# Kernel tuning notes

Hardware: AMD Instinct MI355X
Metric: run time of the kernel (lower is better)

Reference implementation:

```python
import jax, jax.numpy as jnp
import numpy as np

D = 256       # in_channels == hd_channels
H = 8         # heads
HC = D // H   # head dim = 32
NV = 30000    # variables
NC = 60000    # clauses
E = 120000    # edges per polarity


def setup_inputs() -> dict:
    key = jax.random.key(0)
    ks = jax.random.split(key, 16)
    std = 0.02
    v = jax.random.normal(ks[0], (NV, D), jnp.float32)
    c = jax.random.normal(ks[1], (NC, D), jnp.float32)
    # adj row0 indexes clauses (c), row1 indexes variables (v)
    adj_pos = jnp.stack([jax.random.randint(ks[2], (E,), 0, NC),
                         jax.random.randint(ks[3], (E,), 0, NV)]).astype(jnp.int32)
    adj_neg = jnp.stack([jax.random.randint(ks[4], (E,), 0, NC),
                         jax.random.randint(ks[5], (E,), 0, NV)]).astype(jnp.int32)
    # shared projections (ModuleList([lin]*2) shares one module)
    Wq = jax.random.normal(ks[6], (D, D), jnp.float32) * std
    bq = jnp.zeros((D,), jnp.float32)
    Wkv = jax.random.normal(ks[7], (D, 2 * D), jnp.float32) * std
    bkv = jnp.zeros((2 * D,), jnp.float32)
    ffn_v_w1 = jax.random.normal(ks[8], (D, D), jnp.float32) * std
    ffn_v_b1 = jnp.zeros((D,), jnp.float32)
    ffn_v_w2 = jax.random.normal(ks[9], (D, D), jnp.float32) * std
    ffn_v_b2 = jnp.zeros((D,), jnp.float32)
    ffn_c_w1 = jax.random.normal(ks[10], (D, D), jnp.float32) * std
    ffn_c_b1 = jnp.zeros((D,), jnp.float32)
    ffn_c_w2 = jax.random.normal(ks[11], (D, D), jnp.float32) * std
    ffn_c_b2 = jnp.zeros((D,), jnp.float32)
    ones = jnp.ones((D,), jnp.float32)
    zeros = jnp.zeros((D,), jnp.float32)
    return dict(v=v, c=c, adj_pos=adj_pos, adj_neg=adj_neg,
                Wq=Wq, bq=bq, Wkv=Wkv, bkv=bkv,
                ffn_v_w1=ffn_v_w1, ffn_v_b1=ffn_v_b1, ffn_v_w2=ffn_v_w2, ffn_v_b2=ffn_v_b2,
                ffn_c_w1=ffn_c_w1, ffn_c_b1=ffn_c_b1, ffn_c_w2=ffn_c_w2, ffn_c_b2=ffn_c_b2,
                ln_att_v_g=ones, ln_att_v_b=zeros, ln_ffn_v_g=ones, ln_ffn_v_b=zeros,
                ln_att_c_g=ones, ln_att_c_b=zeros, ln_ffn_c_g=ones, ln_ffn_c_b=zeros)


def _split(x):
    return x.reshape(x.shape[0], H, HC)


def _ln(x, g, b, eps=1e-5):
    m = jnp.mean(x, axis=-1, keepdims=True)
    va = jnp.mean(jnp.square(x - m), axis=-1, keepdims=True)
    return (x - m) * jax.lax.rsqrt(va + eps) * g + b


def _seg_softmax(x, seg, n):
    m = jax.ops.segment_max(x, seg, num_segments=n)      # (n, H)
    e = jnp.exp(x - m[seg])
    s = jax.ops.segment_sum(e, seg, num_segments=n)
    return e / s[seg]


def _sparse_attn(q, k, val, e_q, e_k, n_q):
    # q: (Lq,H,HC); k,val: (Lk,H,HC); per-edge dot -> segment softmax -> scatter aggregate
    qk = jnp.einsum('ehc,ehc->eh', q[e_q], k[e_k]) * (1.0 / np.sqrt(HC))
    alpha = _seg_softmax(qk, e_q, n_q)                   # (E,H)
    return jax.ops.segment_sum(alpha[:, :, None] * val[e_k], e_q, num_segments=n_q)


def _cross(x, y, adj, Wq, bq, Wkv, bkv):
    # adj[0] indexes y, adj[1] indexes x
    ey, ex = adj[0], adj[1]
    qx = _split(x @ Wq + bq)
    ky, vy = jnp.split(y @ Wkv + bkv, 2, axis=-1)
    w = _sparse_attn(qx, _split(ky), _split(vy), ex, ey, x.shape[0])   # x queries, transposed edges
    qy = _split(y @ Wq + bq)
    kx, vx = jnp.split(x @ Wkv + bkv, 2, axis=-1)
    u = _sparse_attn(qy, _split(kx), _split(vx), ey, ex, y.shape[0])   # y queries
    return w.reshape(x.shape[0], D), u.reshape(y.shape[0], D)


def _ffn(x, w1, b1, w2, b2):
    return jax.nn.gelu(x @ w1 + b1, approximate=False) @ w2 + b2


def reference(v, c, adj_pos, adj_neg, Wq, bq, Wkv, bkv,
              ffn_v_w1, ffn_v_b1, ffn_v_w2, ffn_v_b2,
              ffn_c_w1, ffn_c_b1, ffn_c_w2, ffn_c_b2,
              ln_att_v_g, ln_att_v_b, ln_ffn_v_g, ln_ffn_v_b,
              ln_att_c_g, ln_att_c_b, ln_ffn_c_g, ln_ffn_c_b):
    wp, up = _cross(v, c, adj_pos, Wq, bq, Wkv, bkv)
    wn, un = _cross(v, c, adj_neg, Wq, bq, Wkv, bkv)
    v1 = _ln(v + (wp + wn), ln_att_v_g, ln_att_v_b)
    c1 = _ln(c + (up + un), ln_att_c_g, ln_att_c_b)
    v2 = _ln(v1 + _ffn(v1, ffn_v_w1, ffn_v_b1, ffn_v_w2, ffn_v_b2), ln_ffn_v_g, ln_ffn_v_b)
    c2 = _ln(c1 + _ffn(c1, ffn_c_w1, ffn_c_b1, ffn_c_w2, ffn_c_b2), ln_ffn_c_g, ln_ffn_c_b)
    return (v2, c2)
```

## Files before the change

### kernel.cpp

```cpp
#include <hip/hip_runtime.h>
#include <math.h>

#define DD 256
#define NH 8

typedef __attribute__((ext_vector_type(8))) short short8;
typedef __attribute__((ext_vector_type(4))) float floatx4;

__device__ __forceinline__ float b2f(unsigned short u) {
    return __uint_as_float(((unsigned)u) << 16);
}
__device__ __forceinline__ unsigned short f2b(float f) {
    unsigned u = __float_as_uint(f);
    return (unsigned short)((u + 0x7fffu + ((u >> 16) & 1u)) >> 16);
}

__device__ __forceinline__ void gload_lds16(const void* g, void* l) {
    __builtin_amdgcn_global_load_lds(
        (const __attribute__((address_space(1))) void*)g,
        (__attribute__((address_space(3))) void*)l, 16, 0, 0);
}

__global__ void detect_dtype(const unsigned* __restrict__ ones_words, int* __restrict__ flag) {
    flag[0] = (ones_words[0] == 0x3F800000u) ? 0 : 1;
}

__device__ __forceinline__ void load8(const void* base, size_t off, int f32, unsigned short* dst) {
    if (f32) {
        const float4* p = (const float4*)((const float*)base + off);
        float4 x = p[0], y = p[1];
        dst[0] = f2b(x.x); dst[1] = f2b(x.y); dst[2] = f2b(x.z); dst[3] = f2b(x.w);
        dst[4] = f2b(y.x); dst[5] = f2b(y.y); dst[6] = f2b(y.z); dst[7] = f2b(y.w);
    } else {
        *(uint4*)dst = *(const uint4*)((const unsigned short*)base + off);
    }
}

__global__ void wt_build(const void* __restrict__ Wq, const void* __restrict__ Wkv,
                         const void* __restrict__ f1v, const void* __restrict__ f1c,
                         const void* __restrict__ f2v, const void* __restrict__ f2c,
                         short* __restrict__ wt, const int* __restrict__ flagp)
{
    const int extf = (*flagp == 0);
    const void* src; int N; size_t dst0;
    switch (blockIdx.z) {
        case 0:  src = Wq;  N = 256; dst0 = 0;          break;
        case 1:  src = Wkv; N = 512; dst0 = 256 * 256;  break;
        case 2:  src = f1v; N = 256; dst0 = 768 * 256;  break;
        case 3:  src = f1c; N = 256; dst0 = 1024 * 256; break;
        case 4:  src = f2v; N = 256; dst0 = 1280 * 256; break;
        default: src = f2c; N = 256; dst0 = 1536 * 256; break;
    }
    int n0 = blockIdx.x * 32, k0 = blockIdx.y * 32;
    if (n0 >= N) return;
    __shared__ short tile[32][33];
    int tx = threadIdx.x & 31, ty = threadIdx.x >> 5;
    #pragma unroll
    for (int i = 0; i < 32; i += 8) {
        int k = k0 + ty + i, n = n0 + tx;
        float val = extf ? ((const float*)src)[(size_t)k * N + n]
                         : b2f(((const unsigned short*)src)[(size_t)k * N + n]);
        tile[ty + i][tx] = (short)f2b(val);
    }
    __syncthreads();
    #pragma unroll
    for (int i = 0; i < 32; i += 8)
        wt[dst0 + (size_t)(n0 + ty + i) * 256 + k0 + tx] = tile[tx][ty + i];
}


__device__ __forceinline__ void stage_b256(const short* wtp, int nbase, int ksub,
                                           char* dstbuf, int wave, int lane)
{
    const char* wb = (const char*)wtp;
    int b = lane & 7;
    #pragma unroll
    for (int i = 0; i < 4; ++i) {
        int r = i * 64 + wave * 8 + (lane >> 3);
        size_t src = (size_t)(nbase + r) * 512 + (size_t)ksub * 128
                   + (size_t)((b * 16) ^ ((r & 7) << 4));
        gload_lds16(wb + src, dstbuf + i * 8192 + wave * 1024);
    }
}

__launch_bounds__(512, 2)
__global__ void proj_gemm5(const void* __restrict__ va, const void* __restrict__ ca,
                           int NVr, int NCr, int bv,
                           const short* __restrict__ wt,
                           const void* __restrict__ bq, const void* __restrict__ bkv,
                           unsigned short* __restrict__ qbuf, unsigned short* __restrict__ kvbuf,
                           const int* __restrict__ flagp)
{
    __shared__ __align__(16) short As[128][264];
    __shared__ __align__(16) char Bs[2][256 * 128];
    const int extf = (*flagp == 0);
    const int t = threadIdx.x;
    const int wave = t >> 6, lane = t & 63;
    const int wm = wave >> 2, wn = wave & 3;
    const int fr = lane & 15, fq = lane >> 4;
    const int bx = blockIdx.x;
    int grow0, nrows, abase_row; const void* asrc;
    if (bx < bv) { grow0 = bx * 128; asrc = va; abase_row = grow0; nrows = NVr - grow0; }
    else { int mc0 = (bx - bv) * 128; grow0 = NVr + mc0; asrc = ca; abase_row = mc0; nrows = NCr - mc0; }
    if (nrows > 128) nrows = 128;

    stage_b256(wt, 0, 0, Bs[0], wave, lane);
    {
        int rbase = t >> 3, cslot = t & 7;
        #pragma unroll
        for (int ii = 0; ii < 8; ++ii) {
            int row = rbase + (ii >> 2) * 64;
            int col = (cslot + (ii & 3) * 8) * 8;
            __align__(16) unsigned short a8[8] = {0, 0, 0, 0, 0, 0, 0, 0};
            if (row < nrows) load8(asrc, (size_t)(abase_row + row) * DD + col, extf, a8);
            *(uint4*)(&As[row][col]) = *(const uint4*)a8;
        }
    }
    __syncthreads();

    int cur = 0;
    for (int c = 0; c < 3; ++c) {
        floatx4 acc[4][4] = {};
        #pragma unroll
        for (int s = 0; s < 4; ++s) {
            int tt = c * 4 + s;
            if (tt + 1 < 12)
                stage_b256(wt, ((tt + 1) >> 2) * 256, (tt + 1) & 3, Bs[cur ^ 1], wave, lane);
            const char* bcur = Bs[cur];
            #pragma unroll
            for (int k32 = 0; k32 < 2; ++k32) {
                short8 afv[4], bfv[4];
                #pragma unroll
                for (int m = 0; m < 4; ++m)
                    afv[m] = *(const short8*)(&As[wm * 64 + m * 16 + fr][s * 64 + k32 * 32 + fq * 8]);
                #pragma unroll
                for (int j = 0; j < 4; ++j) {
                    int rn = wn * 64 + j * 16 + fr;
                    int kb = (k32 * 64 + fq * 16) ^ ((rn & 7) << 4);
                    bfv[j] = *(const short8*)(bcur + rn * 128 + kb);
                }
                #pragma unroll
                for (int m = 0; m < 4; ++m)
                    #pragma unroll
                    for (int j = 0; j < 4; ++j)
                        acc[m][j] = __builtin_amdgcn_mfma_f32_16x16x32_bf16(afv[m], bfv[j], acc[m][j], 0, 0, 0);
            }
            __syncthreads();
            cur ^= 1;
        }
        unsigned short* outp; int ldo, colb; const void* bias;
        if (c == 0) { outp = qbuf;  ldo = 256; colb = 0;             bias = bq;  }
        else        { outp = kvbuf; ldo = 512; colb = (c - 1) * 256; bias = bkv; }
        #pragma unroll
        for (int j = 0; j < 4; ++j) {
            int col = colb + wn * 64 + j * 16 + fr;
            float bvv = extf ? ((const float*)bias)[col] : b2f(((const unsigned short*)bias)[col]);
            #pragma unroll
            for (int m = 0; m < 4; ++m) {
                #pragma unroll
                for (int r = 0; r < 4; ++r) {
                    int rr = wm * 64 + m * 16 + fq * 4 + r;
                    if (rr < nrows)
                        outp[(size_t)(grow0 + rr) * ldo + col] = f2b(acc[m][j][r] + bvv);
                }
            }
        }
    }
}

template<int EPI>
__launch_bounds__(512, 2)
__global__ void ffn_gemm5(const unsigned short* __restrict__ A,
                          int NVr, int NCr, int bv,
                          const short* __restrict__ wtV, const short* __restrict__ wtC,
                          const void* __restrict__ biasV, const void* __restrict__ biasC,
                          void* __restrict__ outp, const int* __restrict__ flagp)
{
    __shared__ __align__(16) short As[128][264];
    __shared__ __align__(16) char Bs[2][256 * 128];
    const int extf = (*flagp == 0);
    const int t = threadIdx.x;
    const int wave = t >> 6, lane = t & 63;
    const int wm = wave >> 2, wn = wave & 3;
    const int fr = lane & 15, fq = lane >> 4;
    const int bx = blockIdx.x;
    int grow0, nrows; const short* wtp; const void* bias;
    if (bx < bv) { grow0 = bx * 128; nrows = NVr - grow0; wtp = wtV; bias = biasV; }
    else { grow0 = NVr + (bx - bv) * 128; nrows = NVr + NCr - grow0; wtp = wtC; bias = biasC; }
    if (nrows > 128) nrows = 128;

    stage_b256(wtp, 0, 0, Bs[0], wave, lane);
    {
        int rbase = t >> 3, cslot = t & 7;
        #pragma unroll
        for (int ii = 0; ii < 8; ++ii) {
            int row = rbase + (ii >> 2) * 64;
            int col = (cslot + (ii & 3) * 8) * 8;
            uint4 a8 = make_uint4(0u, 0u, 0u, 0u);
            if (row < nrows) a8 = *(const uint4*)(A + (size_t)(grow0 + row) * DD + col);
            *(uint4*)(&As[row][col]) = a8;
        }
    }
    __syncthreads();

    int cur = 0;
    floatx4 acc[4][4] = {};
    #pragma unroll
    for (int s = 0; s < 4; ++s) {
        if (s + 1 < 4)
            stage_b256(wtp, 0, s + 1, Bs[cur ^ 1], wave, lane);
        const char* bcur = Bs[cur];
        #pragma unroll
        for (int k32 = 0; k32 < 2; ++k32) {
            short8 afv[4], bfv[4];
            #pragma unroll
            for (int m = 0; m < 4; ++m)
                afv[m] = *(const short8*)(&As[wm * 64 + m * 16 + fr][s * 64 + k32 * 32 + fq * 8]);
            #pragma unroll
            for (int j = 0; j < 4; ++j) {
                int rn = wn * 64 + j * 16 + fr;
                int kb = (k32 * 64 + fq * 16) ^ ((rn & 7) << 4);
                bfv[j] = *(const short8*)(bcur + rn * 128 + kb);
            }
            #pragma unroll
            for (int m = 0; m < 4; ++m)
                #pragma unroll
                for (int j = 0; j < 4; ++j)
                    acc[m][j] = __builtin_amdgcn_mfma_f32_16x16x32_bf16(afv[m], bfv[j], acc[m][j], 0, 0, 0);
        }
        __syncthreads();
        cur ^= 1;
    }
    #pragma unroll
    for (int j = 0; j < 4; ++j) {
        int col = wn * 64 + j * 16 + fr;
        float bvv = extf ? ((const float*)bias)[col] : b2f(((const unsigned short*)bias)[col]);
        #pragma unroll
        for (int m = 0; m < 4; ++m) {
            #pragma unroll
            for (int r = 0; r < 4; ++r) {
                int rr = wm * 64 + m * 16 + fq * 4 + r;
                if (rr < nrows) {
                    float x = acc[m][j][r] + bvv;
                    if (EPI == 1) {
                        x = 0.5f * x * (1.0f + erff(x * 0.70710678118654752f));
                        ((unsigned short*)outp)[(size_t)(grow0 + rr) * DD + col] = f2b(x);
                    } else {
                        ((float*)outp)[(size_t)(grow0 + rr) * DD + col] = x;
                    }
                }
            }
        }
    }
}

__global__ void csr_count(const int* __restrict__ ap, const int* __restrict__ an,
                          int E, int NV, int NT, int* __restrict__ counts) {
    int e = blockIdx.x * 256 + threadIdx.x;
    if (e >= E) return;
    atomicAdd(&counts[ap[E + e]], 1);
    atomicAdd(&counts[NV + ap[e]], 1);
    atomicAdd(&counts[NT + an[E + e]], 1);
    atomicAdd(&counts[NT + NV + an[e]], 1);
}

__global__ void scan_block(const int* __restrict__ counts, int* __restrict__ offs,
                           int* __restrict__ bsum, int n) {
    __shared__ int sm[256];
    int i = blockIdx.x * 256 + threadIdx.x;
    int x = (i < n) ? counts[i] : 0;
    sm[threadIdx.x] = x;
    __syncthreads();
    #pragma unroll
    for (int d = 1; d < 256; d <<= 1) {
        int t = (threadIdx.x >= d) ? sm[threadIdx.x - d] : 0;
        __syncthreads();
        sm[threadIdx.x] += t;
        __syncthreads();
    }
    if (i < n) offs[i] = sm[threadIdx.x] - x;
    if (threadIdx.x == 255) bsum[blockIdx.x] = sm[255];
}

__global__ void scan_bsum(int* __restrict__ bsum, int nb) {
    __shared__ int sm[256];
    __shared__ int carry;
    if (threadIdx.x == 0) carry = 0;
    __syncthreads();
    for (int base = 0; base < nb; base += 256) {
        int i = base + threadIdx.x;
        int x = (i < nb) ? bsum[i] : 0;
        sm[threadIdx.x] = x;
        __syncthreads();
        #pragma unroll
        for (int d = 1; d < 256; d <<= 1) {
            int t = (threadIdx.x >= d) ? sm[threadIdx.x - d] : 0;
            __syncthreads();
            sm[threadIdx.x] += t;
            __syncthreads();
        }
        int excl = sm[threadIdx.x] - x + carry;
        if (i < nb) bsum[i] = excl;
        __syncthreads();
        if (threadIdx.x == 0) carry += sm[255];
        __syncthreads();
    }
}

__global__ void scan_add(int* __restrict__ offs, const int* __restrict__ bsum, int n) {
    int i = blockIdx.x * 256 + threadIdx.x;
    if (i < n) offs[i] += bsum[blockIdx.x];
}

__global__ void csr_fill(const int* __restrict__ ap, const int* __restrict__ an,
                         int E, int NV, int NT, int* __restrict__ offs, int* __restrict__ eids) {
    int e = blockIdx.x * 256 + threadIdx.x;
    if (e >= E) return;
    int p;
    p = atomicAdd(&offs[ap[E + e]], 1);            eids[p] = e * 2;
    p = atomicAdd(&offs[NV + ap[e]], 1);           eids[p] = e * 2 + 1;
    p = atomicAdd(&offs[NT + an[E + e]], 1);       eids[p] = e * 2;
    p = atomicAdd(&offs[NT + NV + an[e]], 1);      eids[p] = e * 2 + 1;
}

__launch_bounds__(256)
__global__ void edge_logits(const int* __restrict__ adj, int E, int NV,
                            const unsigned short* __restrict__ qbuf,
                            const unsigned short* __restrict__ kvbuf,
                            float* __restrict__ qk)
{
    int t = blockIdx.x * 256 + threadIdx.x;
    if (t >= E * 16) return;
    int e = t >> 4, rem = t & 15;
    int dir = rem >> 3, h = rem & 7;
    int ce = adj[e], xe = adj[E + e];
    int qrow = dir ? (NV + ce) : xe;
    int krow = dir ? xe : (NV + ce);
    const unsigned short* qp = qbuf + (size_t)qrow * DD + h * 32;
    const unsigned short* kp = kvbuf + (size_t)krow * 512 + h * 32;
    float s = 0.f;
    #pragma unroll
    for (int i = 0; i < 4; ++i) {
        uint4 qv = ((const uint4*)qp)[i];
        uint4 kv = ((const uint4*)kp)[i];
        const unsigned short* qa = (const unsigned short*)&qv;
        const unsigned short* ka = (const unsigned short*)&kv;
        #pragma unroll
        for (int j = 0; j < 8; ++j) s += b2f(qa[j]) * b2f(ka[j]);
    }
    qk[t] = s * 0.17677669529663689f;
}

__launch_bounds__(256)
__global__ void seg_attn(const int* __restrict__ offs_end, const int* __restrict__ counts,
                         const int* __restrict__ eids, const int* __restrict__ adj,
                         int E, int NV, const float* __restrict__ qk,
                         const unsigned short* __restrict__ kvbuf,
                         float* __restrict__ osum, int NT, int acc_mode)
{
    int seg = blockIdx.x * 4 + (threadIdx.x >> 6);
    if (seg >= NT) return;
    int lane = threadIdx.x & 63;
    int deg = counts[seg];
    float4* op = (float4*)(osum + (size_t)seg * DD) + lane;
    if (deg == 0) {
        if (!acc_mode) *op = make_float4(0.f, 0.f, 0.f, 0.f);
        return;
    }
    int beg = offs_end[seg] - deg;
    int slot = lane >> 3, h = lane & 7;
    float m = -1e30f;
    for (int j = slot; j < deg; j += 8)
        m = fmaxf(m, qk[(size_t)eids[beg + j] * 8 + h]);
    m = fmaxf(m, __shfl_xor(m, 8));
    m = fmaxf(m, __shfl_xor(m, 16));
    m = fmaxf(m, __shfl_xor(m, 32));
    float s = 0.f;
    for (int j = slot; j < deg; j += 8)
        s += __expf(qk[(size_t)eids[beg + j] * 8 + h] - m);
    s += __shfl_xor(s, 8);
    s += __shfl_xor(s, 16);
    s += __shfl_xor(s, 32);
    int h3 = lane >> 3;
    float m3 = __shfl(m, h3);
    float rs3 = 1.f / __shfl(s, h3);
    float a0 = 0.f, a1 = 0.f, a2 = 0.f, a3 = 0.f;
    for (int j = 0; j < deg; ++j) {
        int eid = eids[beg + j];
        int e = eid >> 1, dir = eid & 1;
        int krow = dir ? adj[E + e] : (NV + adj[e]);
        float alpha = __expf(qk[(size_t)eid * 8 + h3] - m3) * rs3;
        ushort4 vv = *(const ushort4*)(kvbuf + (size_t)krow * 512 + DD + lane * 4);
        a0 += alpha * b2f(vv.x);
        a1 += alpha * b2f(vv.y);
        a2 += alpha * b2f(vv.z);
        a3 += alpha * b2f(vv.w);
    }
    float4 o;
    if (acc_mode) {
        float4 old = *op;
        o.x = old.x + a0; o.y = old.y + a1; o.z = old.z + a2; o.w = old.w + a3;
    } else {
        o.x = a0; o.y = a1; o.z = a2; o.w = a3;
    }
    *op = o;
}

template<int BASE_EXT, int OUT_EXT>
__launch_bounds__(256)
__global__ void ln_res(const void* __restrict__ baseA, const void* __restrict__ baseB,
                       const float* __restrict__ add,
                       const void* __restrict__ gA, const void* __restrict__ bA,
                       const void* __restrict__ gB, const void* __restrict__ bB,
                       void* __restrict__ out, int NA, int Ntot, const int* __restrict__ flagp)
{
    int row = blockIdx.x * 4 + (threadIdx.x >> 6);
    if (row >= Ntot) return;
    int lane = threadIdx.x & 63;
    const int extf = (*flagp == 0);
    const void *base, *g, *b;
    size_t roff;
    if (row < NA) { base = baseA; g = gA; b = bA; roff = (size_t)row * DD; }
    else          { base = baseB; g = gB; b = bB; roff = (size_t)(row - NA) * DD; }
    float4 a = ((const float4*)(add + (size_t)row * DD))[lane];
    float y0, y1, y2, y3;
    if (BASE_EXT && extf) {
        float4 t = ((const float4*)((const float*)base + roff))[lane];
        y0 = t.x; y1 = t.y; y2 = t.z; y3 = t.w;
    } else {
        ushort4 t = ((const ushort4*)((const unsigned short*)base + roff))[lane];
        y0 = b2f(t.x); y1 = b2f(t.y); y2 = b2f(t.z); y3 = b2f(t.w);
    }
    y0 += a.x; y1 += a.y; y2 += a.z; y3 += a.w;
    float s = y0 + y1 + y2 + y3;
    #pragma unroll
    for (int off = 32; off; off >>= 1) s += __shfl_xor(s, off);
    float mean = s * (1.0f / DD);
    float d0 = y0 - mean, d1 = y1 - mean, d2 = y2 - mean, d3 = y3 - mean;
    float v = d0 * d0 + d1 * d1 + d2 * d2 + d3 * d3;
    #pragma unroll
    for (int off = 32; off; off >>= 1) v += __shfl_xor(v, off);
    float rstd = rsqrtf(v * (1.0f / DD) + 1e-5f);
    float g0, g1, g2, g3, t0, t1, t2, t3;
    if (extf) {
        float4 gg = ((const float4*)g)[lane]; float4 bt = ((const float4*)b)[lane];
        g0 = gg.x; g1 = gg.y; g2 = gg.z; g3 = gg.w;
        t0 = bt.x; t1 = bt.y; t2 = bt.z; t3 = bt.w;
    } else {
        ushort4 gg = ((const ushort4*)g)[lane]; ushort4 bt = ((const ushort4*)b)[lane];
        g0 = b2f(gg.x); g1 = b2f(gg.y); g2 = b2f(gg.z); g3 = b2f(gg.w);
        t0 = b2f(bt.x); t1 = b2f(bt.y); t2 = b2f(bt.z); t3 = b2f(bt.w);
    }
    float o0 = d0 * rstd * g0 + t0, o1 = d1 * rstd * g1 + t1;
    float o2 = d2 * rstd * g2 + t2, o3 = d3 * rstd * g3 + t3;
    if (OUT_EXT && extf) {
        float4 o; o.x = o0; o.y = o1; o.z = o2; o.w = o3;
        ((float4*)((float*)out + (size_t)row * DD))[lane] = o;
    } else {
        ushort4 o;
        o.x = f2b(o0); o.y = f2b(o1); o.z = f2b(o2); o.w = f2b(o3);
        ((ushort4*)((unsigned short*)out + (size_t)row * DD))[lane] = o;
    }
}

extern "C" void kernel_launch(void* const* d_in, const int* in_sizes, int n_in,
                              void* d_out, int out_size, void* d_ws, size_t ws_size,
                              hipStream_t stream)
{
    const void* v   = d_in[0];
    const void* c   = d_in[1];
    const int* adj_pos = (const int*)d_in[2];
    const int* adj_neg = (const int*)d_in[3];
    const void* Wq  = d_in[4];
    const void* bq  = d_in[5];
    const void* Wkv = d_in[6];
    const void* bkv = d_in[7];
    const void* fvw1 = d_in[8];
    const void* fvb1 = d_in[9];
    const void* fvw2 = d_in[10];
    const void* fvb2 = d_in[11];
    const void* fcw1 = d_in[12];
    const void* fcb1 = d_in[13];
    const void* fcw2 = d_in[14];
    const void* fcb2 = d_in[15];
    const void* lavg = d_in[16];
    const void* lavb = d_in[17];
    const void* lfvg = d_in[18];
    const void* lfvb = d_in[19];
    const void* lacg = d_in[20];
    const void* lacb = d_in[21];
    const void* lfcg = d_in[22];
    const void* lfcb = d_in[23];

    const int NV = in_sizes[0] / DD;
    const int NC = in_sizes[1] / DD;
    const int NT = NV + NC;
    const int E  = in_sizes[2] / 2;

    char* w = (char*)d_ws;
    int* flagp = (int*)w;
    size_t off = 256;
    float* osum = (float*)(w + off);
    off += (size_t)NT * DD * 4;
    unsigned short* qbuf = (unsigned short*)(w + off);
    off += (size_t)NT * DD * 2;
    unsigned short* kvbuf = (unsigned short*)(w + off);
    off += (size_t)NT * DD * 4;
    float* qkbuf = (float*)(w + off);
    off += (size_t)E * 16 * 4;
    int* counts = (int*)(w + off);
    off += (size_t)2 * NT * 4;
    int* offs = (int*)(w + off);
    off += (size_t)2 * NT * 4;
    int* eids = (int*)(w + off);
    off += (size_t)4 * E * 4;
    int* bsum = (int*)(w + off);
    off += 4096;
    short* wt = (short*)(w + off);

    dim3 blk(256), blk512(512);
    const int bv = (NV + 127) / 128, bc = (NC + 127) / 128;
    const int nbE = (E + 255) / 256;
    const int n2 = 2 * NT, nb2 = (n2 + 255) / 256;

    detect_dtype<<<dim3(1), dim3(1), 0, stream>>>((const unsigned*)lavg, flagp);
    wt_build<<<dim3(16, 8, 6), blk, 0, stream>>>(Wq, Wkv, fvw1, fcw1, fvw2, fcw2, wt, flagp);

    proj_gemm5<<<dim3(bv + bc), blk512, 0, stream>>>(v, c, NV, NC, bv, wt, bq, bkv,
                                                     qbuf, kvbuf, flagp);

    hipMemsetAsync(counts, 0, (size_t)n2 * 4, stream);
    csr_count<<<dim3(nbE), blk, 0, stream>>>(adj_pos, adj_neg, E, NV, NT, counts);
    scan_block<<<dim3(nb2), blk, 0, stream>>>(counts, offs, bsum, n2);
    scan_bsum<<<dim3(1), blk, 0, stream>>>(bsum, nb2);
    scan_add<<<dim3(nb2), blk, 0, stream>>>(offs, bsum, n2);
    csr_fill<<<dim3(nbE), blk, 0, stream>>>(adj_pos, adj_neg, E, NV, NT, offs, eids);

    for (int p = 0; p < 2; ++p) {
        const int* adj = p ? adj_neg : adj_pos;
        edge_logits<<<dim3((E * 16 + 255) / 256), blk, 0, stream>>>(adj, E, NV, qbuf, kvbuf, qkbuf);
        seg_attn<<<dim3((NT + 3) / 4), blk, 0, stream>>>(offs + (size_t)p * NT, counts + (size_t)p * NT,
                                                         eids, adj, E, NV, qkbuf, kvbuf, osum, NT, p);
    }

    unsigned short* x1 = qbuf;
    ln_res<1, 0><<<dim3((NT + 3) / 4), blk, 0, stream>>>(v, c, osum, lavg, lavb, lacg, lacb,
                                                         x1, NV, NT, flagp);

    unsigned short* hbuf = kvbuf;
    ffn_gemm5<1><<<dim3(bv + bc), blk512, 0, stream>>>(x1, NV, NC, bv,
                                                       wt + (size_t)768 * 256, wt + (size_t)1024 * 256,
                                                       fvb1, fcb1, hbuf, flagp);
    ffn_gemm5<2><<<dim3(bv + bc), blk512, 0, stream>>>(hbuf, NV, NC, bv,
                                                       wt + (size_t)1280 * 256, wt + (size_t)1536 * 256,
                                                       fvb2, fcb2, osum, flagp);

    ln_res<0, 1><<<dim3((NT + 3) / 4), blk, 0, stream>>>(x1, x1 + (size_t)NV * DD, osum,
                                                         lfvg, lfvb, lfcg, lfcb,
                                                         d_out, NV, NT, flagp);
}
```

Measured before the change: 754.1 us.

## Shrink GEMM tiles to 64 rows with 4 waves and single-buffered XOR-swizzled LDS

The projection and FFN GEMMs now use 64-row tiles with 256 threads instead of 128-row tiles with 512 threads. Each wave covers all 64 rows against its own 64-column slice. The B buffer drops double buffering: the next slice is staged only after a barrier. The A tile gets an XOR swizzle instead of padding, and the MFMA operand order is swapped so each lane holds 4 consecutive columns, allowing vectorized bias loads and packed 8/16-byte stores. The aim is more blocks for occupancy and tail balance and cheaper epilogue stores, at the cost of losing the load/compute overlap from double buffering and staging the weights twice as often per row.

```diff
diff --git a/kernel.cpp b/kernel.cpp
--- a/kernel.cpp
+++ b/kernel.cpp
@@ -69,99 +69,108 @@
 }
 
 
-__device__ __forceinline__ void stage_b256(const short* wtp, int nbase, int ksub,
-                                           char* dstbuf, int wave, int lane)
+__device__ __forceinline__ void stage_b256w4(const short* wtp, int nbase, int ksub,
+                                             char* dstbuf, int wave, int lane)
 {
     const char* wb = (const char*)wtp;
     int b = lane & 7;
     #pragma unroll
-    for (int i = 0; i < 4; ++i) {
-        int r = i * 64 + wave * 8 + (lane >> 3);
+    for (int i = 0; i < 8; ++i) {
+        int r = i * 32 + wave * 8 + (lane >> 3);
         size_t src = (size_t)(nbase + r) * 512 + (size_t)ksub * 128
                    + (size_t)((b * 16) ^ ((r & 7) << 4));
-        gload_lds16(wb + src, dstbuf + i * 8192 + wave * 1024);
-    }
-}
-
-__launch_bounds__(512, 2)
-__global__ void proj_gemm5(const void* __restrict__ va, const void* __restrict__ ca,
+        gload_lds16(wb + src, dstbuf + i * 4096 + wave * 1024);
+    }
+}
+
+__launch_bounds__(256, 2)
+__global__ void proj_gemm7(const void* __restrict__ va, const void* __restrict__ ca,
                            int NVr, int NCr, int bv,
                            const short* __restrict__ wt,
                            const void* __restrict__ bq, const void* __restrict__ bkv,
                            unsigned short* __restrict__ qbuf, unsigned short* __restrict__ kvbuf,
                            const int* __restrict__ flagp)
 {
-    __shared__ __align__(16) short As[128][264];
-    __shared__ __align__(16) char Bs[2][256 * 128];
+    __shared__ __align__(16) char As[64 * 512];
+    __shared__ __align__(16) char Bs[256 * 128];
     const int extf = (*flagp == 0);
     const int t = threadIdx.x;
     const int wave = t >> 6, lane = t & 63;
-    const int wm = wave >> 2, wn = wave & 3;
     const int fr = lane & 15, fq = lane >> 4;
     const int bx = blockIdx.x;
     int grow0, nrows, abase_row; const void* asrc;
-    if (bx < bv) { grow0 = bx * 128; asrc = va; abase_row = grow0; nrows = NVr - grow0; }
-    else { int mc0 = (bx - bv) * 128; grow0 = NVr + mc0; asrc = ca; abase_row = mc0; nrows = NCr - mc0; }
-    if (nrows > 128) nrows = 128;
-
-    stage_b256(wt, 0, 0, Bs[0], wave, lane);
+    if (bx < bv) { grow0 = bx * 64; asrc = va; abase_row = grow0; nrows = NVr - grow0; }
+    else { int mc0 = (bx - bv) * 64; grow0 = NVr + mc0; asrc = ca; abase_row = mc0; nrows = NCr - mc0; }
+    if (nrows > 64) nrows = 64;
+
+    stage_b256w4(wt, 0, 0, Bs, wave, lane);
     {
-        int rbase = t >> 3, cslot = t & 7;
+        int row = t >> 2, cslot = t & 3;
         #pragma unroll
         for (int ii = 0; ii < 8; ++ii) {
-            int row = rbase + (ii >> 2) * 64;
-            int col = (cslot + (ii & 3) * 8) * 8;
+            int colb = cslot * 16 + ii * 64;
+            int swz = colb ^ ((row & 7) << 4);
             __align__(16) unsigned short a8[8] = {0, 0, 0, 0, 0, 0, 0, 0};
-            if (row < nrows) load8(asrc, (size_t)(abase_row + row) * DD + col, extf, a8);
-            *(uint4*)(&As[row][col]) = *(const uint4*)a8;
-        }
-    }
-    __syncthreads();
-
-    int cur = 0;
+            if (row < nrows) load8(asrc, (size_t)(abase_row + row) * DD + colb / 2, extf, a8);
+            *(uint4*)(As + row * 512 + swz) = *(const uint4*)a8;
+        }
+    }
+
+    int tt = 0;
     for (int c = 0; c < 3; ++c) {
         floatx4 acc[4][4] = {};
         #pragma unroll
-        for (int s = 0; s < 4; ++s) {
-            int tt = c * 4 + s;
-            if (tt + 1 < 12)
-                stage_b256(wt, ((tt + 1) >> 2) * 256, (tt + 1) & 3, Bs[cur ^ 1], wave, lane);
-            const char* bcur = Bs[cur];
+        for (int s = 0; s < 4; ++s, ++tt) {
+            __syncthreads();
             #pragma unroll
             for (int k32 = 0; k32 < 2; ++k32) {
                 short8 afv[4], bfv[4];
                 #pragma unroll
-                for (int m = 0; m < 4; ++m)
-                    afv[m] = *(const short8*)(&As[wm * 64 + m * 16 + fr][s * 64 + k32 * 32 + fq * 8]);
+                for (int m = 0; m < 4; ++m) {
+                    int row = m * 16 + fr;
+                    int byt = (s * 128 + k32 * 64 + fq * 16) ^ ((row & 7) << 4);
+                    afv[m] = *(const short8*)(As + row * 512 + byt);
+                }
                 #pragma unroll
                 for (int j = 0; j < 4; ++j) {
-                    int rn = wn * 64 + j * 16 + fr;
+                    int rn = wave * 64 + j * 16 + fr;
                     int kb = (k32 * 64 + fq * 16) ^ ((rn & 7) << 4);
-                    bfv[j] = *(const short8*)(bcur + rn * 128 + kb);
+                    bfv[j] = *(const short8*)(Bs + rn * 128 + kb);
                 }
                 #pragma unroll
                 for (int m = 0; m < 4; ++m)
                     #pragma unroll
                     for (int j = 0; j < 4; ++j)
-                        acc[m][j] = __builtin_amdgcn_mfma_f32_16x16x32_bf16(afv[m], bfv[j], acc[m][j], 0, 0, 0);
+                        acc[m][j] = __builtin_amdgcn_mfma_f32_16x16x32_bf16(bfv[j], afv[m], acc[m][j], 0, 0, 0);
             }
             __syncthreads();
-            cur ^= 1;
-        }
-        unsigned short* outp; int ldo, colb; const void* bias;
-        if (c == 0) { outp = qbuf;  ldo = 256; colb = 0;             bias = bq;  }
-        else        { outp = kvbuf; ldo = 512; colb = (c - 1) * 256; bias = bkv; }
-        #pragma unroll
-        for (int j = 0; j < 4; ++j) {
-            int col = colb + wn * 64 + j * 16 + fr;
-            float bvv = extf ? ((const float*)bias)[col] : b2f(((const unsigned short*)bias)[col]);
-            #pragma unroll
-            for (int m = 0; m < 4; ++m) {
+            if (tt + 1 < 12)
+                stage_b256w4(wt, ((tt + 1) >> 2) * 256, (tt + 1) & 3, Bs, wave, lane);
+        }
+        unsigned short* outp; int ldo, colb0; const void* bias;
+        if (c == 0) { outp = qbuf;  ldo = 256; colb0 = 0;             bias = bq;  }
+        else        { outp = kvbuf; ldo = 512; colb0 = (c - 1) * 256; bias = bkv; }
+        #pragma unroll
+        for (int m = 0; m < 4; ++m) {
+            int row = m * 16 + fr;
+            if (row < nrows) {
+                unsigned short* rp = outp + (size_t)(grow0 + row) * ldo;
                 #pragma unroll
-                for (int r = 0; r < 4; ++r) {
-                    int rr = wm * 64 + m * 16 + fq * 4 + r;
-                    if (rr < nrows)
-                        outp[(size_t)(grow0 + rr) * ldo + col] = f2b(acc[m][j][r] + bvv);
+                for (int j = 0; j < 4; ++j) {
+                    int col = colb0 + wave * 64 + j * 16 + fq * 4;
+                    float b0, b1, b2, b3;
+                    if (extf) {
+                        const float* bp = (const float*)bias + col;
+                        b0 = bp[0]; b1 = bp[1]; b2 = bp[2]; b3 = bp[3];
+                    } else {
+                        const unsigned short* bp = (const unsigned short*)bias + col;
+                        b0 = b2f(bp[0]); b1 = b2f(bp[1]); b2 = b2f(bp[2]); b3 = b2f(bp[3]);
+                    }
+                    float x0 = acc[m][j][0] + b0, x1 = acc[m][j][1] + b1;
+                    float x2 = acc[m][j][2] + b2, x3 = acc[m][j][3] + b3;
+                    unsigned d0 = (unsigned)f2b(x0) | ((unsigned)f2b(x1) << 16);
+                    unsigned d1 = (unsigned)f2b(x2) | ((unsigned)f2b(x3) << 16);
+                    *(uint2*)(rp + col) = make_uint2(d0, d1);
                 }
             }
         }
@@ -169,85 +178,95 @@
 }
 
 template<int EPI>
-__launch_bounds__(512, 2)
-__global__ void ffn_gemm5(const unsigned short* __restrict__ A,
+__launch_bounds__(256, 2)
+__global__ void ffn_gemm7(const unsigned short* __restrict__ A,
                           int NVr, int NCr, int bv,
                           const short* __restrict__ wtV, const short* __restrict__ wtC,
                           const void* __restrict__ biasV, const void* __restrict__ biasC,
                           void* __restrict__ outp, const int* __restrict__ flagp)
 {
-    __shared__ __align__(16) short As[128][264];
-    __shared__ __align__(16) char Bs[2][256 * 128];
+    __shared__ __align__(16) char As[64 * 512];
+    __shared__ __align__(16) char Bs[256 * 128];
     const int extf = (*flagp == 0);
     const int t = threadIdx.x;
     const int wave = t >> 6, lane = t & 63;
-    const int wm = wave >> 2, wn = wave & 3;
     const int fr = lane & 15, fq = lane >> 4;
     const int bx = blockIdx.x;
     int grow0, nrows; const short* wtp; const void* bias;
-    if (bx < bv) { grow0 = bx * 128; nrows = NVr - grow0; wtp = wtV; bias = biasV; }
-    else { grow0 = NVr + (bx - bv) * 128; nrows = NVr + NCr - grow0; wtp = wtC; bias = biasC; }
-    if (nrows > 128) nrows = 128;
-
-    stage_b256(wtp, 0, 0, Bs[0], wave, lane);
+    if (bx < bv) { grow0 = bx * 64; nrows = NVr - grow0; wtp = wtV; bias = biasV; }
+    else { grow0 = NVr + (bx - bv) * 64; nrows = NVr + NCr - grow0; wtp = wtC; bias = biasC; }
+    if (nrows > 64) nrows = 64;
+
+    stage_b256w4(wtp, 0, 0, Bs, wave, lane);
     {
-        int rbase = t >> 3, cslot = t & 7;
+        int row = t >> 2, cslot = t & 3;
         #pragma unroll
         for (int ii = 0; ii < 8; ++ii) {
-            int row = rbase + (ii >> 2) * 64;
-            int col = (cslot + (ii & 3) * 8) * 8;
+            int colb = cslot * 16 + ii * 64;
+            int swz = colb ^ ((row & 7) << 4);
             uint4 a8 = make_uint4(0u, 0u, 0u, 0u);
-            if (row < nrows) a8 = *(const uint4*)(A + (size_t)(grow0 + row) * DD + col);
-            *(uint4*)(&As[row][col]) = a8;
-        }
-    }
-    __syncthreads();
-
-    int cur = 0;
+            if (row < nrows) a8 = *(const uint4*)(A + (size_t)(grow0 + row) * DD + colb / 2);
+            *(uint4*)(As + row * 512 + swz) = a8;
+        }
+    }
+
     floatx4 acc[4][4] = {};
     #pragma unroll
     for (int s = 0; s < 4; ++s) {
-        if (s + 1 < 4)
-            stage_b256(wtp, 0, s + 1, Bs[cur ^ 1], wave, lane);
-        const char* bcur = Bs[cur];
+        __syncthreads();
         #pragma unroll
         for (int k32 = 0; k32 < 2; ++k32) {
             short8 afv[4], bfv[4];
             #pragma unroll
-            for (int m = 0; m < 4; ++m)
-                afv[m] = *(const short8*)(&As[wm * 64 + m * 16 + fr][s * 64 + k32 * 32 + fq * 8]);
+            for (int m = 0; m < 4; ++m) {
+                int row = m * 16 + fr;
+                int byt = (s * 128 + k32 * 64 + fq * 16) ^ ((row & 7) << 4);
+                afv[m] = *(const short8*)(As + row * 512 + byt);
+            }
             #pragma unroll
             for (int j = 0; j < 4; ++j) {
-                int rn = wn * 64 + j * 16 + fr;
+                int rn = wave * 64 + j * 16 + fr;
                 int kb = (k32 * 64 + fq * 16) ^ ((rn & 7) << 4);
-                bfv[j] = *(const short8*)(bcur + rn * 128 + kb);
+                bfv[j] = *(const short8*)(Bs + rn * 128 + kb);
             }
             #pragma unroll
             for (int m = 0; m < 4; ++m)
                 #pragma unroll
                 for (int j = 0; j < 4; ++j)
-                    acc[m][j] = __builtin_amdgcn_mfma_f32_16x16x32_bf16(afv[m], bfv[j], acc[m][j], 0, 0, 0);
-        }
-        __syncthreads();
-        cur ^= 1;
-    }
-    #pragma unroll
-    for (int j = 0; j < 4; ++j) {
-        int col = wn * 64 + j * 16 + fr;
-        float bvv = extf ? ((const float*)bias)[col] : b2f(((const unsigned short*)bias)[col]);
-        #pragma unroll
-        for (int m = 0; m < 4; ++m) {
+                    acc[m][j] = __builtin_amdgcn_mfma_f32_16x16x32_bf16(bfv[j], afv[m], acc[m][j], 0, 0, 0);
+        }
+        __syncthreads();
+        if (s + 1 < 4)
+            stage_b256w4(wtp, 0, s + 1, Bs, wave, lane);
+    }
+    #pragma unroll
+    for (int m = 0; m < 4; ++m) {
+        int row = m * 16 + fr;
+        if (row < nrows) {
             #pragma unroll
-            for (int r = 0; r < 4; ++r) {
-                int rr = wm * 64 + m * 16 + fq * 4 + r;
-                if (rr < nrows) {
-                    float x = acc[m][j][r] + bvv;
-                    if (EPI == 1) {
-                        x = 0.5f * x * (1.0f + erff(x * 0.70710678118654752f));
-                        ((unsigned short*)outp)[(size_t)(grow0 + rr) * DD + col] = f2b(x);
-                    } else {
-                        ((float*)outp)[(size_t)(grow0 + rr) * DD + col] = x;
-                    }
+            for (int j = 0; j < 4; ++j) {
+                int col = wave * 64 + j * 16 + fq * 4;
+                float b0, b1, b2, b3;
+                if (extf) {
+                    const float* bp = (const float*)bias + col;
+                    b0 = bp[0]; b1 = bp[1]; b2 = bp[2]; b3 = bp[3];
+                } else {
+                    const unsigned short* bp = (const unsigned short*)bias + col;
+                    b0 = b2f(bp[0]); b1 = b2f(bp[1]); b2 = b2f(bp[2]); b3 = b2f(bp[3]);
+                }
+                float x0 = acc[m][j][0] + b0, x1 = acc[m][j][1] + b1;
+                float x2 = acc[m][j][2] + b2, x3 = acc[m][j][3] + b3;
+                if (EPI == 1) {
+                    x0 = 0.5f * x0 * (1.0f + erff(x0 * 0.70710678118654752f));
+                    x1 = 0.5f * x1 * (1.0f + erff(x1 * 0.70710678118654752f));
+                    x2 = 0.5f * x2 * (1.0f + erff(x2 * 0.70710678118654752f));
+                    x3 = 0.5f * x3 * (1.0f + erff(x3 * 0.70710678118654752f));
+                    unsigned d0 = (unsigned)f2b(x0) | ((unsigned)f2b(x1) << 16);
+                    unsigned d1 = (unsigned)f2b(x2) | ((unsigned)f2b(x3) << 16);
+                    *(uint2*)((unsigned short*)outp + (size_t)(grow0 + row) * DD + col) = make_uint2(d0, d1);
+                } else {
+                    *(float4*)((float*)outp + (size_t)(grow0 + row) * DD + col)
+                        = make_float4(x0, x1, x2, x3);
                 }
             }
         }
@@ -518,16 +537,16 @@
     off += 4096;
     short* wt = (short*)(w + off);
 
-    dim3 blk(256), blk512(512);
-    const int bv = (NV + 127) / 128, bc = (NC + 127) / 128;
+    dim3 blk(256);
+    const int bv = (NV + 63) / 64, bc = (NC + 63) / 64;
     const int nbE = (E + 255) / 256;
     const int n2 = 2 * NT, nb2 = (n2 + 255) / 256;
 
     detect_dtype<<<dim3(1), dim3(1), 0, stream>>>((const unsigned*)lavg, flagp);
     wt_build<<<dim3(16, 8, 6), blk, 0, stream>>>(Wq, Wkv, fvw1, fcw1, fvw2, fcw2, wt, flagp);
 
-    proj_gemm5<<<dim3(bv + bc), blk512, 0, stream>>>(v, c, NV, NC, bv, wt, bq, bkv,
-                                                     qbuf, kvbuf, flagp);
+    proj_gemm7<<<dim3(bv + bc), blk, 0, stream>>>(v, c, NV, NC, bv, wt, bq, bkv,
+                                                  qbuf, kvbuf, flagp);
 
     hipMemsetAsync(counts, 0, (size_t)n2 * 4, stream);
     csr_count<<<dim3(nbE), blk, 0, stream>>>(adj_pos, adj_neg, E, NV, NT, counts);
@@ -548,12 +567,12 @@
                                                          x1, NV, NT, flagp);
 
     unsigned short* hbuf = kvbuf;
-    ffn_gemm5<1><<<dim3(bv + bc), blk512, 0, stream>>>(x1, NV, NC, bv,
-                                                       wt + (size_t)768 * 256, wt + (size_t)1024 * 256,
-                                                       fvb1, fcb1, hbuf, flagp);
-    ffn_gemm5<2><<<dim3(bv + bc), blk512, 0, stream>>>(hbuf, NV, NC, bv,
-                                                       wt + (size_t)1280 * 256, wt + (size_t)1536 * 256,
-                                                       fvb2, fcb2, osum, flagp);
+    ffn_gemm7<1><<<dim3(bv + bc), blk, 0, stream>>>(x1, NV, NC, bv,
+                                                    wt + (size_t)768 * 256, wt + (size_t)1024 * 256,
+                                                    fvb1, fcb1, hbuf, flagp);
+    ffn_gemm7<2><<<dim3(bv + bc), blk, 0, stream>>>(hbuf, NV, NC, bv,
+                                                    wt + (size_t)1280 * 256, wt + (size_t)1536 * 256,
+                                                    fvb2, fcb2, osum, flagp);
 
     ln_res<0, 1><<<dim3((NT + 3) / 4), blk, 0, stream>>>(x1, x1 + (size_t)NV * DD, osum,
                                                          lfvg, lfvb, lfcg, lfcb,
```

New measurement: 713.6 us. 5.4% less time.
